# Performance work log

Hardware: AMD Instinct MI355X
Metric: run time of the kernel (lower is better)

## Reference

```python
import jax, jax.numpy as jnp
import numpy as np

B, IN, H = 4096, 2048, 2048

def hard_sigmoid(x):
    # torch nn.Hardsigmoid / QHardSigmoid: clip(x/6 + 0.5, 0, 1)
    return jnp.clip(x / 6.0 + 0.5, 0.0, 1.0)

def hard_tanh(x):
    return jnp.clip(x, -1.0, 1.0)

def setup_inputs() -> dict:
    key = jax.random.key(0)
    k1, k2, k3, k4, k5 = jax.random.split(key, 5)
    return {
        "input_": jax.random.normal(k1, (B, IN), dtype=jnp.float32),
        "h_0": jax.random.normal(k2, (B, H), dtype=jnp.float32),
        "c_0": jax.random.normal(k3, (B, H), dtype=jnp.float32),
        "W_ih": jax.random.normal(k4, (4 * H, IN), dtype=jnp.float32) * (1.0 / np.sqrt(IN)),
        "W_hh": jax.random.normal(k5, (4 * H, H), dtype=jnp.float32) * (1.0 / np.sqrt(H)),
        "b_hh": jnp.zeros((4 * H,), dtype=jnp.float32),
    }

def reference(input_, h_0, c_0, W_ih, W_hh, b_hh):
    # Two GEMMs: x @ W_ih^T (no bias) and h @ W_hh^T + b
    wi = jnp.einsum('bi,gi->bg', input_, W_ih)          # [B, 4H]
    wh_b = jnp.einsum('bh,gh->bg', h_0, W_hh) + b_hh     # [B, 4H]
    h_x4 = wh_b + wi
    f, i, o, g = jnp.split(h_x4, 4, axis=1)              # split order: f, i, o, g
    new = hard_sigmoid(i) * hard_tanh(g)
    old = hard_sigmoid(f) * c_0
    c_1 = old + new
    h_1 = hard_sigmoid(o) * hard_tanh(c_1)
    return (h_1, c_1)
```

## Files before the change

kernel.cpp:

```cpp
#include <hip/hip_runtime.h>
#include <hip/hip_bf16.h>


typedef __attribute__((ext_vector_type(8))) short short8;
typedef __attribute__((ext_vector_type(4))) float f32x4;

#define B_SZ 4096
#define K_SZ 4096
#define N_SZ 8192
#define H_SZ 2048

typedef const __attribute__((address_space(1))) void gvoid_t;
typedef __attribute__((address_space(3))) void lvoid_t;

__device__ __forceinline__ void gload_lds16(const __hip_bfloat16* g, void* l) {
    __builtin_amdgcn_global_load_lds((gvoid_t*)g, (lvoid_t*)l, 16, 0, 0);
}

__device__ __forceinline__ float hsig(float x) {
    return fminf(fmaxf(x * (1.0f / 6.0f) + 0.5f, 0.0f), 1.0f);
}
__device__ __forceinline__ float htanh(float x) {
    return fminf(fmaxf(x, -1.0f), 1.0f);
}

__global__ void cvt_concat_kernel(const float* __restrict__ a,
                                  const float* __restrict__ b,
                                  __hip_bfloat16* __restrict__ out,
                                  int total4)
{
    int i = blockIdx.x * blockDim.x + threadIdx.x;
    if (i >= total4) return;
    int idx = i << 2;
    int r = idx >> 12;
    int c = idx & 4095;
    const float* src = (c < 2048) ? (a + (size_t)r * 2048 + c)
                                  : (b + (size_t)r * 2048 + (c - 2048));
    float4 v = *reinterpret_cast<const float4*>(src);
    union { ushort4 u; __hip_bfloat16 h[4]; } p;
    p.h[0] = __float2bfloat16(v.x);
    p.h[1] = __float2bfloat16(v.y);
    p.h[2] = __float2bfloat16(v.z);
    p.h[3] = __float2bfloat16(v.w);
    *reinterpret_cast<ushort4*>(out + idx) = p.u;
}

__global__ void cvt_w_perm_kernel(const float* __restrict__ wih,
                                  const float* __restrict__ whh,
                                  __hip_bfloat16* __restrict__ out,
                                  int total4)
{
    int i = blockIdx.x * blockDim.x + threadIdx.x;
    if (i >= total4) return;
    int idx = i << 2;
    int r = idx >> 12;
    int c = idx & 4095;
    int gate = (r >> 4) & 3;
    int j = ((r >> 6) << 4) | (r & 15);
    int srow = gate * 2048 + j;
    const float* src = (c < 2048) ? (wih + (size_t)srow * 2048 + c)
                                  : (whh + (size_t)srow * 2048 + (c - 2048));
    float4 v = *reinterpret_cast<const float4*>(src);
    union { ushort4 u; __hip_bfloat16 h[4]; } p;
    p.h[0] = __float2bfloat16(v.x);
    p.h[1] = __float2bfloat16(v.y);
    p.h[2] = __float2bfloat16(v.z);
    p.h[3] = __float2bfloat16(v.w);
    *reinterpret_cast<ushort4*>(out + idx) = p.u;
}

__global__ __launch_bounds__(256)
void gemm_fused_kernel(const __hip_bfloat16* __restrict__ A,
                       const __hip_bfloat16* __restrict__ Bw,
                       const float* __restrict__ c0,
                       const float* __restrict__ bias,
                       float* __restrict__ out)
{
    constexpr int BM = 128, BN = 128, BK = 64;
    constexpr int NBM = B_SZ / BM;
    constexpr int NBN = N_SZ / BN;
    constexpr int NWG = NBM * NBN;
    constexpr int ABYTES = BM * BK * 2;

    __shared__ __align__(16) char lds[2 * ABYTES];

    const int tid  = threadIdx.x;
    const int wave = tid >> 6;
    const int lane = tid & 63;
    const int wr = wave >> 1, wc = wave & 1;
    const int fr  = lane & 15;
    const int fkq = lane >> 4;

    int bid = blockIdx.x;
    int swz = (bid & 7) * (NWG / 8) + (bid >> 3);
    int bm = swz / NBN, bn = swz % NBN;

    const int rs = tid >> 3;
    const int ch = tid & 7;
    const int lch = ch ^ (rs & 7);
    const __hip_bfloat16* pa = A  + (size_t)(bm * BM + rs) * K_SZ + lch * 8;
    const __hip_bfloat16* pb = Bw + (size_t)(bn * BN + rs) * K_SZ + lch * 8;

    int a_off[4], b_off[4];
#pragma unroll
    for (int m = 0; m < 4; ++m) {
        int row = wr * 64 + m * 16 + fr;
        a_off[m] = row * 128 + ((fkq ^ (row & 7)) << 4);
    }
#pragma unroll
    for (int n = 0; n < 4; ++n) {
        int row = wc * 64 + n * 16 + fr;
        b_off[n] = row * 128 + ((fkq ^ (row & 7)) << 4);
    }

    f32x4 acc[4][4];
#pragma unroll
    for (int m = 0; m < 4; ++m)
#pragma unroll
        for (int n = 0; n < 4; ++n)
            acc[m][n] = f32x4{0.f, 0.f, 0.f, 0.f};

    for (int kt = 0; kt < K_SZ; kt += BK) {
#pragma unroll
        for (int s = 0; s < 4; ++s)
            gload_lds16(pa + (size_t)s * 32 * K_SZ + kt, lds + s * 4096 + wave * 1024);
#pragma unroll
        for (int s = 0; s < 4; ++s)
            gload_lds16(pb + (size_t)s * 32 * K_SZ + kt, lds + ABYTES + s * 4096 + wave * 1024);
        __syncthreads();

        short8 av[4], bv[4];
#pragma unroll
        for (int kk = 0; kk < 2; ++kk) {
            const int x = kk * 64;
#pragma unroll
            for (int m = 0; m < 4; ++m) av[m] = *(const short8*)(lds + (a_off[m] ^ x));
#pragma unroll
            for (int n = 0; n < 4; ++n) bv[n] = *(const short8*)(lds + ABYTES + (b_off[n] ^ x));
#pragma unroll
            for (int m = 0; m < 4; ++m)
#pragma unroll
                for (int n = 0; n < 4; ++n)
                    acc[m][n] = __builtin_amdgcn_mfma_f32_16x16x32_bf16(av[m], bv[n], acc[m][n], 0, 0, 0);
        }
        __syncthreads();
    }

    const int jj = (bn * 2 + wc) * 16 + fr;
    const float bf = bias[jj];
    const float bi = bias[2048 + jj];
    const float bo = bias[4096 + jj];
    const float bg = bias[6144 + jj];
    const int row0 = bm * BM + wr * 64 + fkq * 4;
    float* h1out = out;
    float* c1out = out + (size_t)B_SZ * H_SZ;
#pragma unroll
    for (int m = 0; m < 4; ++m) {
#pragma unroll
        for (int i = 0; i < 4; ++i) {
            int r = row0 + m * 16 + i;
            float c0v = c0[(size_t)r * H_SZ + jj];
            float f  = acc[m][0][i] + bf;
            float ig = acc[m][1][i] + bi;
            float o  = acc[m][2][i] + bo;
            float g  = acc[m][3][i] + bg;
            float cn = hsig(f) * c0v + hsig(ig) * htanh(g);
            h1out[(size_t)r * H_SZ + jj] = hsig(o) * htanh(cn);
            c1out[(size_t)r * H_SZ + jj] = cn;
        }
    }
}

extern "C" void kernel_launch(void* const* d_in, const int* in_sizes, int n_in,
                              void* d_out, int out_size, void* d_ws, size_t ws_size,
                              hipStream_t stream)
{
    const float* x   = (const float*)d_in[0];
    const float* h0  = (const float*)d_in[1];
    const float* c0  = (const float*)d_in[2];
    const float* Wih = (const float*)d_in[3];
    const float* Whh = (const float*)d_in[4];
    const float* bhh = (const float*)d_in[5];
    float* out = (float*)d_out;

    if (ws_size < (size_t)96 * 1024 * 1024) return;
    char* ws = (char*)d_ws;
    __hip_bfloat16* Xp = (__hip_bfloat16*)ws;
    __hip_bfloat16* Wp = (__hip_bfloat16*)(ws + (size_t)32 * 1024 * 1024);

    int t4x = B_SZ * K_SZ / 4;
    cvt_concat_kernel<<<t4x / 256, 256, 0, stream>>>(x, h0, Xp, t4x);
    int t4w = N_SZ * K_SZ / 4;
    cvt_w_perm_kernel<<<t4w / 256, 256, 0, stream>>>(Wih, Whh, Wp, t4w);

    gemm_fused_kernel<<<2048, 256, 0, stream>>>(Xp, Wp, c0, bhh, out);
}
```

Before: 579.1 us.

## Use 256x256 tiles with double-buffered LDS and interleaved load/MFMA phases

Replaces the 128x128, single-buffered, 4-wave GEMM with a 256x256 tile computed by 8 waves. It uses 128 KB of dynamic LDS for double buffering and splits each K-step into four sub-phases, so global-to-LDS loads for the next tile are issued while MFMAs run on the current one. The sub-phases are gated with explicit waitcnt, barriers and setprio. The weight permutation kernel is changed so each 64-column block of gates lines up with the new wave layout for the fused LSTM epilogue. The aim is to hide memory latency and raise data reuse per tile. The costs are higher register pressure, fewer workgroups (512), and reliance on hand-placed waitcnt counts being correct.

```diff
diff --git a/kernel.cpp b/kernel.cpp
--- a/kernel.cpp
+++ b/kernel.cpp
@@ -55,8 +55,8 @@
     int idx = i << 2;
     int r = idx >> 12;
     int c = idx & 4095;
-    int gate = (r >> 4) & 3;
-    int j = ((r >> 6) << 4) | (r & 15);
+    int gate = (((r >> 7) & 1) << 1) | ((r >> 4) & 1);
+    int j = (r & 15) | (((r >> 5) & 3) << 4) | ((r >> 8) << 6);
     int srow = gate * 2048 + j;
     const float* src = (c < 2048) ? (wih + (size_t)srow * 2048 + c)
                                   : (whh + (size_t)srow * 2048 + (c - 2048));
@@ -69,106 +69,206 @@
     *reinterpret_cast<ushort4*>(out + idx) = p.u;
 }
 
-__global__ __launch_bounds__(256)
+__global__ __launch_bounds__(512, 2)
 void gemm_fused_kernel(const __hip_bfloat16* __restrict__ A,
                        const __hip_bfloat16* __restrict__ Bw,
                        const float* __restrict__ c0,
                        const float* __restrict__ bias,
                        float* __restrict__ out)
 {
-    constexpr int BM = 128, BN = 128, BK = 64;
-    constexpr int NBM = B_SZ / BM;
-    constexpr int NBN = N_SZ / BN;
-    constexpr int NWG = NBM * NBN;
-    constexpr int ABYTES = BM * BK * 2;
-
-    __shared__ __align__(16) char lds[2 * ABYTES];
+    constexpr int BK = 64;
+    constexpr int NT = K_SZ / BK;
+    constexpr int NWG = (B_SZ / 256) * (N_SZ / 256);
+    constexpr int TILEB = 65536;
+
+    extern __shared__ __align__(16) char lds[];
 
     const int tid  = threadIdx.x;
     const int wave = tid >> 6;
     const int lane = tid & 63;
-    const int wr = wave >> 1, wc = wave & 1;
-    const int fr  = lane & 15;
-    const int fkq = lane >> 4;
+    const int wrow = wave >> 2;
+    const int wcol = wave & 3;
+    const int fr   = lane & 15;
+    const int fkq  = lane >> 4;
 
     int bid = blockIdx.x;
     int swz = (bid & 7) * (NWG / 8) + (bid >> 3);
-    int bm = swz / NBN, bn = swz % NBN;
-
-    const int rs = tid >> 3;
-    const int ch = tid & 7;
+    int bm = swz >> 5;
+    int bn = swz & 31;
+
+    const int rs  = tid >> 3;
+    const int ch  = tid & 7;
     const int lch = ch ^ (rs & 7);
-    const __hip_bfloat16* pa = A  + (size_t)(bm * BM + rs) * K_SZ + lch * 8;
-    const __hip_bfloat16* pb = Bw + (size_t)(bn * BN + rs) * K_SZ + lch * 8;
-
-    int a_off[4], b_off[4];
-#pragma unroll
-    for (int m = 0; m < 4; ++m) {
-        int row = wr * 64 + m * 16 + fr;
-        a_off[m] = row * 128 + ((fkq ^ (row & 7)) << 4);
-    }
-#pragma unroll
-    for (int n = 0; n < 4; ++n) {
-        int row = wc * 64 + n * 16 + fr;
-        b_off[n] = row * 128 + ((fkq ^ (row & 7)) << 4);
-    }
-
-    f32x4 acc[4][4];
-#pragma unroll
-    for (int m = 0; m < 4; ++m)
+    const __hip_bfloat16* pa = A  + (size_t)(bm * 256 + rs) * K_SZ + lch * 8;
+    const __hip_bfloat16* pb = Bw + (size_t)(bn * 256 + rs) * K_SZ + lch * 8;
+
+#define STG_A(bufn, kt, srow) \
+    gload_lds16(pa + (size_t)(srow) * K_SZ + (kt), (bufn) + (srow) * 128 + wave * 1024)
+#define STG_B(bufn, kt, srow) \
+    gload_lds16(pb + (size_t)(srow) * K_SZ + (kt), (bufn) + 32768 + (srow) * 128 + wave * 1024)
+
+    int a_off[4], b_off[2];
+#pragma unroll
+    for (int mf = 0; mf < 4; ++mf) {
+        int row = wrow * 64 + mf * 16 + fr;
+        a_off[mf] = row * 128 + ((fkq ^ (row & 7)) << 4);
+    }
+#pragma unroll
+    for (int nf = 0; nf < 2; ++nf) {
+        int row = wcol * 32 + nf * 16 + fr;
+        b_off[nf] = row * 128 + ((fkq ^ (row & 7)) << 4);
+    }
+
+    f32x4 acc[8][4];
+#pragma unroll
+    for (int m = 0; m < 8; ++m)
 #pragma unroll
         for (int n = 0; n < 4; ++n)
             acc[m][n] = f32x4{0.f, 0.f, 0.f, 0.f};
 
-    for (int kt = 0; kt < K_SZ; kt += BK) {
-#pragma unroll
-        for (int s = 0; s < 4; ++s)
-            gload_lds16(pa + (size_t)s * 32 * K_SZ + kt, lds + s * 4096 + wave * 1024);
-#pragma unroll
-        for (int s = 0; s < 4; ++s)
-            gload_lds16(pb + (size_t)s * 32 * K_SZ + kt, lds + ABYTES + s * 4096 + wave * 1024);
-        __syncthreads();
-
-        short8 av[4], bv[4];
-#pragma unroll
-        for (int kk = 0; kk < 2; ++kk) {
-            const int x = kk * 64;
-#pragma unroll
-            for (int m = 0; m < 4; ++m) av[m] = *(const short8*)(lds + (a_off[m] ^ x));
-#pragma unroll
-            for (int n = 0; n < 4; ++n) bv[n] = *(const short8*)(lds + ABYTES + (b_off[n] ^ x));
-#pragma unroll
-            for (int m = 0; m < 4; ++m)
-#pragma unroll
-                for (int n = 0; n < 4; ++n)
-                    acc[m][n] = __builtin_amdgcn_mfma_f32_16x16x32_bf16(av[m], bv[n], acc[m][n], 0, 0, 0);
-        }
-        __syncthreads();
-    }
-
-    const int jj = (bn * 2 + wc) * 16 + fr;
+    {
+        char* b0 = lds;
+        STG_A(b0, 0, 0);   STG_A(b0, 0, 64);
+        STG_B(b0, 0, 0);   STG_B(b0, 0, 64);
+        STG_A(b0, 0, 128); STG_A(b0, 0, 192);
+        STG_B(b0, 0, 128); STG_B(b0, 0, 192);
+    }
+    asm volatile("s_waitcnt vmcnt(4)" ::: "memory");
+    asm volatile("s_barrier" ::: "memory");
+
+    short8 av[4][2], bv[2][2];
+
+#pragma unroll 1
+    for (int t = 0; t < NT; ++t) {
+        char* bufc = lds + (t & 1) * TILEB;
+        char* bufn = lds + ((t + 1) & 1) * TILEB;
+        const char* Ab = bufc;
+        const char* Bb = bufc + 32768;
+        const int ktn = (t + 1) * BK;
+        const bool st = (t + 1 < NT);
+
+#pragma unroll
+        for (int mf = 0; mf < 4; ++mf)
+#pragma unroll
+            for (int ks = 0; ks < 2; ++ks)
+                av[mf][ks] = *(const short8*)(Ab + (a_off[mf] ^ (ks << 6)));
+#pragma unroll
+        for (int nf = 0; nf < 2; ++nf)
+#pragma unroll
+            for (int ks = 0; ks < 2; ++ks)
+                bv[nf][ks] = *(const short8*)(Bb + (b_off[nf] ^ (ks << 6)));
+        if (st) { STG_A(bufn, ktn, 0); STG_A(bufn, ktn, 64); }
+        asm volatile("s_barrier" ::: "memory");
+        asm volatile("s_waitcnt lgkmcnt(0)" ::: "memory");
+        __builtin_amdgcn_sched_barrier(0);
+        __builtin_amdgcn_s_setprio(1);
+#pragma unroll
+        for (int mf = 0; mf < 4; ++mf)
+#pragma unroll
+            for (int nf = 0; nf < 2; ++nf)
+#pragma unroll
+                for (int ks = 0; ks < 2; ++ks)
+                    acc[mf][nf] = __builtin_amdgcn_mfma_f32_16x16x32_bf16(av[mf][ks], bv[nf][ks], acc[mf][nf], 0, 0, 0);
+        __builtin_amdgcn_s_setprio(0);
+        if (st) asm volatile("s_waitcnt vmcnt(2)" ::: "memory");
+        else    asm volatile("s_waitcnt vmcnt(0)" ::: "memory");
+        asm volatile("s_barrier" ::: "memory");
+
+#pragma unroll
+        for (int nf = 0; nf < 2; ++nf)
+#pragma unroll
+            for (int ks = 0; ks < 2; ++ks)
+                bv[nf][ks] = *(const short8*)(Bb + 16384 + (b_off[nf] ^ (ks << 6)));
+        if (st) { STG_B(bufn, ktn, 0); STG_B(bufn, ktn, 64); }
+        asm volatile("s_barrier" ::: "memory");
+        asm volatile("s_waitcnt lgkmcnt(0)" ::: "memory");
+        __builtin_amdgcn_sched_barrier(0);
+        __builtin_amdgcn_s_setprio(1);
+#pragma unroll
+        for (int mf = 0; mf < 4; ++mf)
+#pragma unroll
+            for (int nf = 0; nf < 2; ++nf)
+#pragma unroll
+                for (int ks = 0; ks < 2; ++ks)
+                    acc[mf][2 + nf] = __builtin_amdgcn_mfma_f32_16x16x32_bf16(av[mf][ks], bv[nf][ks], acc[mf][2 + nf], 0, 0, 0);
+        __builtin_amdgcn_s_setprio(0);
+        asm volatile("s_barrier" ::: "memory");
+
+#pragma unroll
+        for (int mf = 0; mf < 4; ++mf)
+#pragma unroll
+            for (int ks = 0; ks < 2; ++ks)
+                av[mf][ks] = *(const short8*)(Ab + 16384 + (a_off[mf] ^ (ks << 6)));
+#pragma unroll
+        for (int nf = 0; nf < 2; ++nf)
+#pragma unroll
+            for (int ks = 0; ks < 2; ++ks)
+                bv[nf][ks] = *(const short8*)(Bb + (b_off[nf] ^ (ks << 6)));
+        if (st) { STG_A(bufn, ktn, 128); STG_A(bufn, ktn, 192); }
+        asm volatile("s_barrier" ::: "memory");
+        asm volatile("s_waitcnt lgkmcnt(0)" ::: "memory");
+        __builtin_amdgcn_sched_barrier(0);
+        __builtin_amdgcn_s_setprio(1);
+#pragma unroll
+        for (int mf = 0; mf < 4; ++mf)
+#pragma unroll
+            for (int nf = 0; nf < 2; ++nf)
+#pragma unroll
+                for (int ks = 0; ks < 2; ++ks)
+                    acc[4 + mf][nf] = __builtin_amdgcn_mfma_f32_16x16x32_bf16(av[mf][ks], bv[nf][ks], acc[4 + mf][nf], 0, 0, 0);
+        __builtin_amdgcn_s_setprio(0);
+        asm volatile("s_barrier" ::: "memory");
+
+#pragma unroll
+        for (int nf = 0; nf < 2; ++nf)
+#pragma unroll
+            for (int ks = 0; ks < 2; ++ks)
+                bv[nf][ks] = *(const short8*)(Bb + 16384 + (b_off[nf] ^ (ks << 6)));
+        if (st) { STG_B(bufn, ktn, 128); STG_B(bufn, ktn, 192); }
+        asm volatile("s_barrier" ::: "memory");
+        asm volatile("s_waitcnt lgkmcnt(0)" ::: "memory");
+        __builtin_amdgcn_sched_barrier(0);
+        __builtin_amdgcn_s_setprio(1);
+#pragma unroll
+        for (int mf = 0; mf < 4; ++mf)
+#pragma unroll
+            for (int nf = 0; nf < 2; ++nf)
+#pragma unroll
+                for (int ks = 0; ks < 2; ++ks)
+                    acc[4 + mf][2 + nf] = __builtin_amdgcn_mfma_f32_16x16x32_bf16(av[mf][ks], bv[nf][ks], acc[4 + mf][2 + nf], 0, 0, 0);
+        __builtin_amdgcn_s_setprio(0);
+        if (st) asm volatile("s_waitcnt vmcnt(4)" ::: "memory");
+        asm volatile("s_barrier" ::: "memory");
+    }
+#undef STG_A
+#undef STG_B
+
+    const int jj = bn * 64 + wcol * 16 + fr;
     const float bf = bias[jj];
     const float bi = bias[2048 + jj];
     const float bo = bias[4096 + jj];
     const float bg = bias[6144 + jj];
-    const int row0 = bm * BM + wr * 64 + fkq * 4;
     float* h1out = out;
     float* c1out = out + (size_t)B_SZ * H_SZ;
 #pragma unroll
-    for (int m = 0; m < 4; ++m) {
-#pragma unroll
-        for (int i = 0; i < 4; ++i) {
-            int r = row0 + m * 16 + i;
-            float c0v = c0[(size_t)r * H_SZ + jj];
-            float f  = acc[m][0][i] + bf;
-            float ig = acc[m][1][i] + bi;
-            float o  = acc[m][2][i] + bo;
-            float g  = acc[m][3][i] + bg;
-            float cn = hsig(f) * c0v + hsig(ig) * htanh(g);
-            h1out[(size_t)r * H_SZ + jj] = hsig(o) * htanh(cn);
-            c1out[(size_t)r * H_SZ + jj] = cn;
+    for (int mh = 0; mh < 2; ++mh)
+#pragma unroll
+        for (int mf = 0; mf < 4; ++mf) {
+            const int m = mh * 4 + mf;
+            const int row0 = bm * 256 + mh * 128 + wrow * 64 + mf * 16 + fkq * 4;
+#pragma unroll
+            for (int i = 0; i < 4; ++i) {
+                int r = row0 + i;
+                float c0v = c0[(size_t)r * H_SZ + jj];
+                float f  = acc[m][0][i] + bf;
+                float ig = acc[m][1][i] + bi;
+                float o  = acc[m][2][i] + bo;
+                float g  = acc[m][3][i] + bg;
+                float cn = hsig(f) * c0v + hsig(ig) * htanh(g);
+                h1out[(size_t)r * H_SZ + jj] = hsig(o) * htanh(cn);
+                c1out[(size_t)r * H_SZ + jj] = cn;
+            }
         }
-    }
 }
 
 extern "C" void kernel_launch(void* const* d_in, const int* in_sizes, int n_in,
@@ -193,5 +293,5 @@
     int t4w = N_SZ * K_SZ / 4;
     cvt_w_perm_kernel<<<t4w / 256, 256, 0, stream>>>(Wih, Whh, Wp, t4w);
 
-    gemm_fused_kernel<<<2048, 256, 0, stream>>>(Xp, Wp, c0, bhh, out);
-}
+    gemm_fused_kernel<<<512, 512, 131072, stream>>>(Xp, Wp, c0, bhh, out);
+}
```

Result: faster. 480.4 us (-17.0%).
